# Kernel tuning notes

Hardware: AMD Instinct MI355X
Metric: run time of the kernel (lower is better)

The kernel has to match this reference:

```python
import jax, jax.numpy as jnp
import numpy as np

N, E, D, H = 50000, 500000, 128, 128


def setup_inputs() -> dict:
    key = jax.random.key(0)
    ks = jax.random.split(key, 20)
    s = 0.05
    inp = {
        "node_states": jax.random.normal(ks[0], (N, D), jnp.float32),
        "edge_features": jax.random.normal(ks[1], (E, D), jnp.float32),
        "from_idx": jax.random.randint(ks[2], (E,), 0, N, dtype=jnp.int32),
        "to_idx": jax.random.randint(ks[3], (E,), 0, N, dtype=jnp.int32),
        "graph_idx": jax.random.randint(ks[4], (N,), 0, 16, dtype=jnp.int32),
        # message MLP: Linear(3D,H)-ReLU-Linear(H,H)-ReLU-Linear(H,D)
        "mW1": jax.random.normal(ks[5], (3 * D, H), jnp.float32) * s,
        "mb1": jnp.zeros((H,), jnp.float32),
        "mW2": jax.random.normal(ks[6], (H, H), jnp.float32) * s,
        "mb2": jnp.zeros((H,), jnp.float32),
        "mW3": jax.random.normal(ks[7], (H, D), jnp.float32) * s,
        "mb3": jnp.zeros((D,), jnp.float32),
    }
    # three GRU cells; W: input->gates [D,3D], U: hidden->gates [D,3D]; gate order r,z,n (torch)
    for i, g in enumerate(["g0", "g1", "g2"]):
        inp[g + "W"] = jax.random.normal(ks[8 + 2 * i], (D, 3 * D), jnp.float32) * s
        inp[g + "U"] = jax.random.normal(ks[9 + 2 * i], (D, 3 * D), jnp.float32) * s
        inp[g + "b"] = jnp.zeros((3 * D,), jnp.float32)
        inp[g + "c"] = jnp.zeros((3 * D,), jnp.float32)
    return inp


def _mlp(x, W1, b1, W2, b2, W3, b3):
    h = jax.nn.relu(x @ W1 + b1)
    h = jax.nn.relu(h @ W2 + b2)
    return h @ W3 + b3


def _gru(x, h, W, U, b, c):
    gi = x @ W + b  # [N,3D]
    gh = h @ U + c
    ir, iz, inn = jnp.split(gi, 3, axis=1)
    hr, hz, hn = jnp.split(gh, 3, axis=1)
    r = jax.nn.sigmoid(ir + hr)
    z = jax.nn.sigmoid(iz + hz)
    n = jnp.tanh(inn + r * hn)
    return (1.0 - z) * n + z * h


def reference(node_states, edge_features, from_idx, to_idx, graph_idx,
              mW1, mb1, mW2, mb2, mW3, mb3,
              g0W, g0U, g0b, g0c, g1W, g1U, g1b, g1c, g2W, g2U, g2b, g2c):
    n_nodes = node_states.shape[0]

    def prop_once(fi, ti):
        edge_in = jnp.concatenate(
            [node_states[fi], node_states[ti], edge_features], axis=1)  # [E,3D]
        edge_states = _mlp(edge_in, mW1, mb1, mW2, mb2, mW3, mb3)  # [E,D]
        return jax.ops.segment_sum(edge_states, ti, num_segments=n_nodes)

    # forward uses self.message_net for BOTH directions (reverse net unused)
    agg = prop_once(from_idx, to_idx) + prop_once(to_idx, from_idx)  # [N,D]

    h1 = _gru(node_states, agg, g0W, g0U, g0b, g0c)
    h2 = _gru(agg, h1, g1W, g1U, g1b, g1c)
    h3 = _gru(h1, h2, g2W, g2U, g2b, g2c)
    return h3
```

## Files before the change

### kernel.cpp

```cpp
#include <hip/hip_runtime.h>

typedef unsigned short u16;
typedef __attribute__((ext_vector_type(8))) short bf16x8;
typedef __attribute__((ext_vector_type(4))) float f32x4;

__device__ inline u16 f2bf(float f) {
  unsigned int u = __float_as_uint(f);
  u += 0x7fffu + ((u >> 16) & 1u);
  return (u16)(u >> 16);
}
__device__ inline float bf2f(u16 v) {
  return __uint_as_float((unsigned)v << 16);
}

__device__ inline uint4 pack8(float4 a, float4 b) {
  uint4 r;
  r.x = (unsigned)f2bf(a.x) | ((unsigned)f2bf(a.y) << 16);
  r.y = (unsigned)f2bf(a.z) | ((unsigned)f2bf(a.w) << 16);
  r.z = (unsigned)f2bf(b.x) | ((unsigned)f2bf(b.y) << 16);
  r.w = (unsigned)f2bf(b.z) | ((unsigned)f2bf(b.w) << 16);
  return r;
}

__device__ inline void atomic_pk_add_bf16(u16* p, unsigned v) {
  asm volatile("global_atomic_pk_add_bf16 %0, %1, off" : : "v"(p), "v"(v)
               : "memory");
}

struct TransDesc {
  const float* src[9];
  u16* dst[9];
  int R[9];
  int C[9];
  int pre[10];
};

__global__ void transpose_all_kernel(TransDesc td) {
  int t = blockIdx.x * 256 + threadIdx.x;
  if (t >= td.pre[9]) return;
  int seg = 0;
  while (t >= td.pre[seg + 1]) ++seg;
  int local = t - td.pre[seg];
  int C = td.C[seg], R = td.R[seg];
  int r = local / C, c = local - r * C;
  td.dst[seg][(size_t)c * R + r] = f2bf(td.src[seg][local]);
}

__global__ void bf16_to_f32_kernel(const u16* __restrict__ in,
                                   float* __restrict__ out, int n8) {
  int t = blockIdx.x * 256 + threadIdx.x;
  if (t < n8) {
    uint4 v = ((const uint4*)in)[t];
    u16* p = (u16*)&v;
    float4 o0 = {bf2f(p[0]), bf2f(p[1]), bf2f(p[2]), bf2f(p[3])};
    float4 o1 = {bf2f(p[4]), bf2f(p[5]), bf2f(p[6]), bf2f(p[7])};
    ((float4*)out)[t * 2] = o0;
    ((float4*)out)[t * 2 + 1] = o1;
  }
}

__global__ void count_kernel(const int* __restrict__ fi,
                             const int* __restrict__ ti,
                             int* __restrict__ cnt, int E) {
  int e = blockIdx.x * 256 + threadIdx.x;
  if (e < E) {
    atomicAdd(&cnt[ti[e]], 1);
    atomicAdd(&cnt[fi[e]], 1);
  }
}

__global__ void scan1_kernel(const int* __restrict__ cnt,
                             int* __restrict__ partial, int N, int chunk) {
  __shared__ int sdata[256];
  int b = blockIdx.x, t = threadIdx.x;
  int base = b * chunk;
  int sum = 0;
  for (int i = t; i < chunk; i += 256) {
    int idx = base + i;
    if (idx < N) sum += cnt[idx];
  }
  sdata[t] = sum;
  __syncthreads();
  for (int s2 = 128; s2 > 0; s2 >>= 1) {
    if (t < s2) sdata[t] += sdata[t + s2];
    __syncthreads();
  }
  if (t == 0) partial[b] = sdata[0];
}

__global__ void scan2_kernel(int* __restrict__ partial, int* __restrict__ off,
                             int N) {
  __shared__ int s[256];
  int t = threadIdx.x;
  int own = partial[t];
  s[t] = own;
  __syncthreads();
  for (int d2 = 1; d2 < 256; d2 <<= 1) {
    int v = (t >= d2) ? s[t - d2] : 0;
    __syncthreads();
    s[t] += v;
    __syncthreads();
  }
  partial[t] = s[t] - own;
  if (t == 255) off[N] = s[255];
}

__global__ void scan3_kernel(const int* __restrict__ cnt,
                             const int* __restrict__ partialEx,
                             int* __restrict__ off, int* __restrict__ cursor,
                             int N, int chunk) {
  __shared__ int s[256];
  int b = blockIdx.x, t = threadIdx.x;
  int base = b * chunk;
  int own = (t < chunk && base + t < N) ? cnt[base + t] : 0;
  s[t] = own;
  __syncthreads();
  for (int d2 = 1; d2 < 256; d2 <<= 1) {
    int v = (t >= d2) ? s[t - d2] : 0;
    __syncthreads();
    s[t] += v;
    __syncthreads();
  }
  int ex = s[t] - own + partialEx[b];
  if (t < chunk && base + t < N) {
    off[base + t] = ex;
    cursor[base + t] = ex;
  }
}

__global__ void pos_kernel(const int* __restrict__ fi,
                           const int* __restrict__ ti, int* __restrict__ cursor,
                           int* __restrict__ pos0, int* __restrict__ pos1,
                           int E) {
  int e = blockIdx.x * 256 + threadIdx.x;
  if (e < E) {
    pos0[e] = atomicAdd(&cursor[ti[e]], 1);
    pos1[e] = atomicAdd(&cursor[fi[e]], 1);
  }
}

__global__ __launch_bounds__(256) void agg_csr_kernel(
    const u16* __restrict__ msg, const int* __restrict__ off,
    float* __restrict__ aggf, int N) {
  int n = blockIdx.x * 4 + (threadIdx.x >> 6);
  if (n >= N) return;
  int lane = threadIdx.x & 63;
  int s = off[n], e = off[n + 1];
  float a0 = 0.f, a1 = 0.f, b0 = 0.f, b1 = 0.f;
  const unsigned* m32 = (const unsigned*)msg;
  int r = s;
  for (; r + 1 < e; r += 2) {
    unsigned d0 = m32[(size_t)r * 64 + lane];
    unsigned d1 = m32[(size_t)(r + 1) * 64 + lane];
    a0 += bf2f((u16)(d0 & 0xffff));
    a1 += bf2f((u16)(d0 >> 16));
    b0 += bf2f((u16)(d1 & 0xffff));
    b1 += bf2f((u16)(d1 >> 16));
  }
  if (r < e) {
    unsigned d0 = m32[(size_t)r * 64 + lane];
    a0 += bf2f((u16)(d0 & 0xffff));
    a1 += bf2f((u16)(d0 >> 16));
  }
  aggf[(size_t)n * 128 + lane * 2] = a0 + b0;
  aggf[(size_t)n * 128 + lane * 2 + 1] = a1 + b1;
}

__device__ inline void stage_w_rw(u16* sW, const u16* __restrict__ src,
                                  int roww, int colofs, int tid) {
  int n = tid >> 1, half = tid & 1;
  const u16* s = src + (size_t)n * roww + colofs + half * 64;
#pragma unroll
  for (int q = 0; q < 8; ++q) {
    uint4 v = *(const uint4*)(s + q * 8);
    int byte = n * 256 + ((half * 128 + q * 16) ^ ((n & 7) << 4));
    *(uint4*)((char*)sW + byte) = v;
  }
}

__device__ inline void mfma_pass(const u16* A, const u16* W, f32x4 acc[8],
                                 int w, int lane) {
  const int cA = lane & 15;
  const int ko = (lane >> 4) * 8;
  const int arow = 16 * w + cA;
#pragma unroll
  for (int kk = 0; kk < 4; ++kk) {
    int ka = (kk * 32 + ko) * 2;
    int sx = ka ^ ((cA & 7) << 4);
    bf16x8 a = *(const bf16x8*)((const char*)A + arow * 256 + sx);
#pragma unroll
    for (int nt = 0; nt < 8; ++nt) {
      bf16x8 bb = *(const bf16x8*)((const char*)W + (nt * 16 + cA) * 256 + sx);
      acc[nt] = __builtin_amdgcn_mfma_f32_16x16x32_bf16(a, bb, acc[nt], 0, 0, 0);
    }
  }
}

__device__ inline void write_h_lds(u16* sH, const f32x4 acc[8], int w,
                                   int lane) {
#pragma unroll
  for (int nt = 0; nt < 8; ++nt) {
    int col = nt * 16 + (lane & 15);
#pragma unroll
    for (int i = 0; i < 4; ++i) {
      int rr = 16 * w + ((lane >> 4) * 4) + i;
      *(u16*)((char*)sH + rr * 256 + ((col * 2) ^ ((rr & 7) << 4))) =
          f2bf(acc[nt][i]);
    }
  }
}

__device__ inline void stage_w_512(u16* sW, const u16* __restrict__ src,
                                   int roww, int colofs, int tid) {
  int n = tid >> 2, quarter = tid & 3;
  const u16* s = src + (size_t)n * roww + colofs + quarter * 32;
#pragma unroll
  for (int q = 0; q < 4; ++q) {
    uint4 v = *(const uint4*)(s + q * 8);
    int byte = n * 256 + ((quarter * 64 + q * 16) ^ ((n & 7) << 4));
    *(uint4*)((char*)sW + byte) = v;
  }
}

__global__ __launch_bounds__(256) void node_partial_kernel(
    const float* __restrict__ ns, const u16* __restrict__ Wt1,
    u16* __restrict__ Pa, u16* __restrict__ Pb, int N) {
  __shared__ u16 sA[64 * 128];
  __shared__ u16 sW[128 * 128];
  const int tid = threadIdx.x;
  const int lane = tid & 63;
  const int w = tid >> 6;
  const int r0 = blockIdx.x * 64;
  {
    int row = tid >> 2, seg = tid & 3;
    int rr = r0 + row;
    if (rr >= N) rr = N - 1;
    const float4* sx = (const float4*)(ns + (size_t)rr * 128 + seg * 32);
#pragma unroll
    for (int q = 0; q < 4; ++q) {
      int byte = row * 256 + ((seg * 64 + q * 16) ^ ((row & 7) << 4));
      *(uint4*)((char*)sA + byte) = pack8(sx[q * 2], sx[q * 2 + 1]);
    }
  }
  stage_w_rw(sW, Wt1, 384, 0, tid);
  __syncthreads();
  f32x4 accA[8] = {};
  mfma_pass(sA, sW, accA, w, lane);
  __syncthreads();
  stage_w_rw(sW, Wt1, 384, 128, tid);
  __syncthreads();
  f32x4 accB[8] = {};
  mfma_pass(sA, sW, accB, w, lane);
#pragma unroll
  for (int nt = 0; nt < 8; ++nt) {
    int col = nt * 16 + (lane & 15);
#pragma unroll
    for (int i = 0; i < 4; ++i) {
      int rr = 16 * w + ((lane >> 4) * 4) + i;
      int row = r0 + rr;
      if (row < N) {
        Pa[(size_t)row * 128 + col] = f2bf(accA[nt][i]);
        Pb[(size_t)row * 128 + col] = f2bf(accB[nt][i]);
      }
    }
  }
}

template <int MODE>
__global__ __launch_bounds__(512, 2) void edge_fused_kernel(
    const float* __restrict__ ef, const int* __restrict__ from_idx,
    const int* __restrict__ to_idx, const u16* __restrict__ Wt1,
    const u16* __restrict__ Wt2, const u16* __restrict__ Wt3,
    const u16* __restrict__ Pa, const u16* __restrict__ Pb,
    const float* __restrict__ b1, const float* __restrict__ b2,
    const float* __restrict__ b3, const int* __restrict__ pos0,
    const int* __restrict__ pos1, u16* __restrict__ out_buf, int E,
    int ntiles) {
  __shared__ u16 sW1c[128 * 128];
  __shared__ u16 sH[128 * 128];
  __shared__ int sPos[128];
  const int tid = threadIdx.x;
  const int lane = tid & 63;
  const int wv = tid >> 6;
  const int mw = wv >> 1;
  const int nw = wv & 1;
  const int dir = mw >> 1;
  const int l15 = lane & 15;
  const int lhi = lane >> 4;

  stage_w_512(sW1c, Wt1, 384, 256, tid);

  float b1f[4], b2f[4], b3f[4];
#pragma unroll
  for (int nt = 0; nt < 4; ++nt) {
    int col = (nw << 6) + (nt << 4) + l15;
    b1f[nt] = b1[col];
    b2f[nt] = b2[col];
    b3f[nt] = b3[col];
  }
  bf16x8 w2f[4][4], w3f[4][4];
#pragma unroll
  for (int nt = 0; nt < 4; ++nt) {
    int c = (nw << 6) + (nt << 4) + l15;
#pragma unroll
    for (int kk = 0; kk < 4; ++kk) {
      w2f[nt][kk] = *(const bf16x8*)(Wt2 + (size_t)c * 128 + (kk << 5) + (lhi << 3));
      w3f[nt][kk] = *(const bf16x8*)(Wt3 + (size_t)c * 128 + (kk << 5) + (lhi << 3));
    }
  }
  __syncthreads();

  for (int t = blockIdx.x; t < ntiles; t += gridDim.x) {
    const int e0 = t << 6;
    if (MODE == 0 && tid < 128) {
      int er = tid & 63;
      int e = e0 + er;
      int p = -1;
      if (e < E) p = (tid < 64) ? pos0[e] : pos1[e];
      sPos[tid] = p;
    }
    {
      const int arow = (mw << 4) + l15;
      int e = e0 + arow;
      if (e >= E) e = E - 1;
      const float* ep = ef + (size_t)e * 128 + (lhi << 3);
      bf16x8 efA[4];
#pragma unroll
      for (int kk = 0; kk < 4; ++kk) {
        float4 f0 = *(const float4*)(ep + (kk << 5));
        float4 f1 = *(const float4*)(ep + (kk << 5) + 4);
        uint4 u = pack8(f0, f1);
        efA[kk] = *(bf16x8*)&u;
      }
      f32x4 a1[4] = {};
#pragma unroll
      for (int kk = 0; kk < 4; ++kk) {
#pragma unroll
        for (int nt = 0; nt < 4; ++nt) {
          int c = (nw << 6) + (nt << 4) + l15;
          int sx = ((kk << 6) + (lhi << 4)) ^ ((c & 7) << 4);
          bf16x8 bb = *(const bf16x8*)((const char*)sW1c + c * 256 + sx);
          a1[nt] = __builtin_amdgcn_mfma_f32_16x16x32_bf16(efA[kk], bb, a1[nt], 0, 0, 0);
        }
      }
#pragma unroll
      for (int nt = 0; nt < 4; ++nt) {
        int col = (nw << 6) + (nt << 4) + l15;
#pragma unroll
        for (int i = 0; i < 4; ++i) {
          int row = (mw << 4) + (lhi << 2) + i;
          u16 val = f2bf(a1[nt][i] + b1f[nt]);
          int sw = (col * 2) ^ ((row & 7) << 4);
          *(u16*)((char*)sH + row * 256 + sw) = val;
          *(u16*)((char*)sH + (row + 64) * 256 + sw) = val;
        }
      }
    }
    __syncthreads();
#pragma unroll
    for (int it = 0; it < 4; ++it) {
      int row = (tid >> 4) + (it << 5);
      int c8 = tid & 15;
      int er = row & 63, d = row >> 6;
      int ec = e0 + er;
      if (ec >= E) ec = E - 1;
      int fi_e = from_idx[ec], ti_e = to_idx[ec];
      int sA = d ? ti_e : fi_e;
      int sB = d ? fi_e : ti_e;
      char* hptr = (char*)sH + row * 256 + ((c8 << 4) ^ ((row & 7) << 4));
      uint4 efv = *(const uint4*)hptr;
      uint4 pav = *(const uint4*)(Pa + (size_t)sA * 128 + (c8 << 3));
      uint4 pbv = *(const uint4*)(Pb + (size_t)sB * 128 + (c8 << 3));
      const u16* pe = (const u16*)&efv;
      const u16* pa = (const u16*)&pav;
      const u16* pb = (const u16*)&pbv;
      unsigned o[4];
#pragma unroll
      for (int j = 0; j < 4; ++j) {
        float v0 = fmaxf(bf2f(pe[2 * j]) + bf2f(pa[2 * j]) + bf2f(pb[2 * j]), 0.f);
        float v1 = fmaxf(bf2f(pe[2 * j + 1]) + bf2f(pa[2 * j + 1]) + bf2f(pb[2 * j + 1]), 0.f);
        o[j] = (unsigned)f2bf(v0) | ((unsigned)f2bf(v1) << 16);
      }
      *(uint4*)hptr = *(uint4*)o;
    }
    __syncthreads();
    bf16x8 hA[2][4];
#pragma unroll
    for (int m = 0; m < 2; ++m) {
      int ra = (mw << 5) + (m << 4) + l15;
#pragma unroll
      for (int kk = 0; kk < 4; ++kk) {
        int sx = ((kk << 6) + (lhi << 4)) ^ ((ra & 7) << 4);
        hA[m][kk] = *(const bf16x8*)((const char*)sH + ra * 256 + sx);
      }
    }
    f32x4 acc2[2][4] = {};
#pragma unroll
    for (int kk = 0; kk < 4; ++kk)
#pragma unroll
      for (int nt = 0; nt < 4; ++nt)
#pragma unroll
        for (int m = 0; m < 2; ++m)
          acc2[m][nt] = __builtin_amdgcn_mfma_f32_16x16x32_bf16(
              hA[m][kk], w2f[nt][kk], acc2[m][nt], 0, 0, 0);
    __syncthreads();
#pragma unroll
    for (int m = 0; m < 2; ++m) {
#pragma unroll
      for (int i = 0; i < 4; ++i) {
        int rl = (mw << 5) + (m << 4) + (lhi << 2) + i;
#pragma unroll
        for (int nt = 0; nt < 4; ++nt) {
          int col = (nw << 6) + (nt << 4) + l15;
          float v = fmaxf(acc2[m][nt][i] + b2f[nt], 0.f);
          *(u16*)((char*)sH + rl * 256 + ((col * 2) ^ ((rl & 7) << 4))) = f2bf(v);
        }
      }
    }
    __syncthreads();
#pragma unroll
    for (int m = 0; m < 2; ++m) {
      int ra = (mw << 5) + (m << 4) + l15;
#pragma unroll
      for (int kk = 0; kk < 4; ++kk) {
        int sx = ((kk << 6) + (lhi << 4)) ^ ((ra & 7) << 4);
        hA[m][kk] = *(const bf16x8*)((const char*)sH + ra * 256 + sx);
      }
    }
    f32x4 acc3[2][4] = {};
#pragma unroll
    for (int kk = 0; kk < 4; ++kk)
#pragma unroll
      for (int nt = 0; nt < 4; ++nt)
#pragma unroll
        for (int m = 0; m < 2; ++m)
          acc3[m][nt] = __builtin_amdgcn_mfma_f32_16x16x32_bf16(
              hA[m][kk], w3f[nt][kk], acc3[m][nt], 0, 0, 0);

    if (MODE == 0) {
      __syncthreads();
#pragma unroll
      for (int m = 0; m < 2; ++m) {
#pragma unroll
        for (int i = 0; i < 4; ++i) {
          int rl = (mw << 5) + (m << 4) + (lhi << 2) + i;
#pragma unroll
          for (int nt = 0; nt < 4; ++nt) {
            int col = (nw << 6) + (nt << 4) + l15;
            *(u16*)((char*)sH + rl * 256 + ((col * 2) ^ ((rl & 7) << 4))) =
                f2bf(acc3[m][nt][i] + b3f[nt]);
          }
        }
      }
      __syncthreads();
#pragma unroll
      for (int it = 0; it < 4; ++it) {
        int task = tid + (it << 9);
        int row = task >> 4, c8 = task & 15;
        int p = sPos[row];
        if (p >= 0) {
          uint4 v = *(const uint4*)((const char*)sH + row * 256 +
                                    ((c8 << 4) ^ ((row & 7) << 4)));
          *(uint4*)(out_buf + (size_t)p * 128 + (c8 << 3)) = v;
        }
      }
      __syncthreads();
    } else {
#pragma unroll
      for (int m = 0; m < 2; ++m) {
#pragma unroll
        for (int i = 0; i < 4; ++i) {
          int er = ((mw & 1) << 5) + (m << 4) + (lhi << 2) + i;
          int e = e0 + er;
#pragma unroll
          for (int nt = 0; nt < 4; ++nt) {
            int col = (nw << 6) + (nt << 4) + l15;
            float v = acc3[m][nt][i] + b3f[nt];
            float vp = __shfl_xor(v, 1);
            if (e < E && !(lane & 1)) {
              int dest = dir ? from_idx[e] : to_idx[e];
              unsigned d2 = (unsigned)f2bf(v) | ((unsigned)f2bf(vp) << 16);
              atomic_pk_add_bf16(out_buf + (size_t)dest * 128 + col, d2);
            }
          }
        }
      }
      __syncthreads();
    }
  }
}

__global__ __launch_bounds__(256, 2) void gru3_kernel(
    const float* __restrict__ ns, const float* __restrict__ aggf,
    const u16* __restrict__ g0W, const u16* __restrict__ g0U,
    const u16* __restrict__ g1W, const u16* __restrict__ g1U,
    const u16* __restrict__ g2W, const u16* __restrict__ g2U,
    const float* __restrict__ b0, const float* __restrict__ c0,
    const float* __restrict__ b1, const float* __restrict__ c1,
    const float* __restrict__ b2, const float* __restrict__ c2,
    float* __restrict__ out, int N) {
  __shared__ u16 sX[64 * 128];
  __shared__ u16 sG[64 * 128];
  __shared__ u16 sW[128 * 128];
  const int tid = threadIdx.x;
  const int lane = tid & 63;
  const int w = tid >> 6;
  const int r0 = blockIdx.x * 64;
  {
    int row = tid >> 2, seg = tid & 3;
    int rr = r0 + row;
    if (rr >= N) rr = N - 1;
    const float4* sx = (const float4*)(ns + (size_t)rr * 128 + seg * 32);
    const float4* sh = (const float4*)(aggf + (size_t)rr * 128 + seg * 32);
#pragma unroll
    for (int q = 0; q < 4; ++q) {
      int byte = row * 256 + ((seg * 64 + q * 16) ^ ((row & 7) << 4));
      *(uint4*)((char*)sX + byte) = pack8(sx[q * 2], sx[q * 2 + 1]);
      *(uint4*)((char*)sG + byte) = pack8(sh[q * 2], sh[q * 2 + 1]);
    }
  }

  float hpf[8][4];

#define GPASS(SRC, ABUF, ACC)                       \
  __syncthreads();                                  \
  stage_w_rw(sW, (SRC), 128, 0, tid);               \
  __syncthreads();                                  \
  mfma_pass((ABUF), sW, (ACC), w, lane);

  {
    f32x4 ar[8] = {}, az[8] = {}, ai[8] = {}, ah[8] = {};
    GPASS(g0W + 0 * 16384, sX, ar)
    GPASS(g0U + 0 * 16384, sG, ar)
    GPASS(g0W + 1 * 16384, sX, az)
    GPASS(g0U + 1 * 16384, sG, az)
    GPASS(g0W + 2 * 16384, sX, ai)
    GPASS(g0U + 2 * 16384, sG, ah)
    f32x4 h1[8];
#pragma unroll
    for (int nt = 0; nt < 8; ++nt) {
      int col = nt * 16 + (lane & 15);
      float brc = b0[col] + c0[col];
      float bzc = b0[128 + col] + c0[128 + col];
      float bi = b0[256 + col];
      float bc2 = c0[256 + col];
#pragma unroll
      for (int i = 0; i < 4; ++i) {
        int rloc = 16 * w + ((lane >> 4) * 4) + i;
        int row = r0 + rloc;
        int rowc = row < N ? row : N - 1;
        float hf = aggf[(size_t)rowc * 128 + col];
        float rg = 1.f / (1.f + __expf(-(ar[nt][i] + brc)));
        float zg = 1.f / (1.f + __expf(-(az[nt][i] + bzc)));
        float pre = ai[nt][i] + bi + rg * (ah[nt][i] + bc2);
        float ng = 2.f / (1.f + __expf(-2.f * pre)) - 1.f;
        float hv = (1.f - zg) * ng + zg * hf;
        h1[nt][i] = hv;
        hpf[nt][i] = hv;
      }
    }
    write_h_lds(sX, h1, w, lane);
  }
  {
    f32x4 ar[8] = {}, az[8] = {}, ai[8] = {}, ah[8] = {};
    GPASS(g1W + 0 * 16384, sG, ar)
    GPASS(g1U + 0 * 16384, sX, ar)
    GPASS(g1W + 1 * 16384, sG, az)
    GPASS(g1U + 1 * 16384, sX, az)
    GPASS(g1W + 2 * 16384, sG, ai)
    GPASS(g1U + 2 * 16384, sX, ah)
    f32x4 h2[8];
#pragma unroll
    for (int nt = 0; nt < 8; ++nt) {
      int col = nt * 16 + (lane & 15);
      float brc = b1[col] + c1[col];
      float bzc = b1[128 + col] + c1[128 + col];
      float bi = b1[256 + col];
      float bc2 = c1[256 + col];
#pragma unroll
      for (int i = 0; i < 4; ++i) {
        float rg = 1.f / (1.f + __expf(-(ar[nt][i] + brc)));
        float zg = 1.f / (1.f + __expf(-(az[nt][i] + bzc)));
        float pre = ai[nt][i] + bi + rg * (ah[nt][i] + bc2);
        float ng = 2.f / (1.f + __expf(-2.f * pre)) - 1.f;
        float hv = (1.f - zg) * ng + zg * hpf[nt][i];
        h2[nt][i] = hv;
        hpf[nt][i] = hv;
      }
    }
    write_h_lds(sG, h2, w, lane);
  }
  {
    f32x4 ar[8] = {}, az[8] = {}, ai[8] = {}, ah[8] = {};
    GPASS(g2W + 0 * 16384, sX, ar)
    GPASS(g2U + 0 * 16384, sG, ar)
    GPASS(g2W + 1 * 16384, sX, az)
    GPASS(g2U + 1 * 16384, sG, az)
    GPASS(g2W + 2 * 16384, sX, ai)
    GPASS(g2U + 2 * 16384, sG, ah)
#pragma unroll
    for (int nt = 0; nt < 8; ++nt) {
      int col = nt * 16 + (lane & 15);
      float brc = b2[col] + c2[col];
      float bzc = b2[128 + col] + c2[128 + col];
      float bi = b2[256 + col];
      float bc2 = c2[256 + col];
#pragma unroll
      for (int i = 0; i < 4; ++i) {
        int rloc = 16 * w + ((lane >> 4) * 4) + i;
        int row = r0 + rloc;
        if (row < N) {
          float rg = 1.f / (1.f + __expf(-(ar[nt][i] + brc)));
          float zg = 1.f / (1.f + __expf(-(az[nt][i] + bzc)));
          float pre = ai[nt][i] + bi + rg * (ah[nt][i] + bc2);
          float ng = 2.f / (1.f + __expf(-2.f * pre)) - 1.f;
          out[(size_t)row * 128 + col] = (1.f - zg) * ng + zg * hpf[nt][i];
        }
      }
    }
  }
#undef GPASS
}

extern "C" void kernel_launch(void* const* d_in, const int* in_sizes, int n_in,
                              void* d_out, int out_size, void* d_ws,
                              size_t ws_size, hipStream_t stream) {
  const float* ns = (const float*)d_in[0];
  const float* ef = (const float*)d_in[1];
  const int* from_idx = (const int*)d_in[2];
  const int* to_idx = (const int*)d_in[3];
  const float* mW1 = (const float*)d_in[5];
  const float* mb1 = (const float*)d_in[6];
  const float* mW2 = (const float*)d_in[7];
  const float* mb2 = (const float*)d_in[8];
  const float* mW3 = (const float*)d_in[9];
  const float* mb3 = (const float*)d_in[10];
  const float* gW[3] = {(const float*)d_in[11], (const float*)d_in[15], (const float*)d_in[19]};
  const float* gU[3] = {(const float*)d_in[12], (const float*)d_in[16], (const float*)d_in[20]};
  const float* gb[3] = {(const float*)d_in[13], (const float*)d_in[17], (const float*)d_in[21]};
  const float* gc[3] = {(const float*)d_in[14], (const float*)d_in[18], (const float*)d_in[22]};

  const int N = in_sizes[0] / 128;
  const int E = in_sizes[1] / 128;

  char* base = (char*)d_ws;
  size_t cur = 0;
  auto alloc = [&](size_t bytes) {
    size_t p = cur;
    cur = (cur + bytes + 255) & ~(size_t)255;
    return (void*)(base + p);
  };
  float* aggf = (float*)alloc((size_t)N * 128 * 4);
  u16* Pa = (u16*)alloc((size_t)N * 128 * 2);
  u16* Pb = (u16*)alloc((size_t)N * 128 * 2);
  u16* Wt1 = (u16*)alloc(384 * 128 * 2);
  u16* Wt2 = (u16*)alloc(128 * 128 * 2);
  u16* Wt3 = (u16*)alloc(128 * 128 * 2);
  u16 *gWt[3], *gUt[3];
  for (int i = 0; i < 3; ++i) {
    gWt[i] = (u16*)alloc(384 * 128 * 2);
    gUt[i] = (u16*)alloc(384 * 128 * 2);
  }
  int* cnt = (int*)alloc((size_t)N * 4);
  int* off = (int*)alloc((size_t)(N + 1) * 4);
  int* cursor = (int*)alloc((size_t)N * 4);
  int* partial = (int*)alloc(256 * 4);
  int* pos0 = (int*)alloc((size_t)E * 4);
  int* pos1 = (int*)alloc((size_t)E * 4);
  u16* aggb = (u16*)alloc((size_t)N * 128 * 2);
  u16* msg = (u16*)alloc((size_t)2 * E * 128 * 2);
  bool csr_ok = (cur <= ws_size);

  {
    TransDesc td;
    const float* srcs[9] = {mW1, mW2, mW3, gW[0], gU[0], gW[1], gU[1], gW[2], gU[2]};
    u16* dsts[9] = {Wt1, Wt2, Wt3, gWt[0], gUt[0], gWt[1], gUt[1], gWt[2], gUt[2]};
    int Rs[9] = {384, 128, 128, 128, 128, 128, 128, 128, 128};
    int Cs[9] = {128, 128, 128, 384, 384, 384, 384, 384, 384};
    int acc = 0;
    for (int i = 0; i < 9; ++i) {
      td.src[i] = srcs[i];
      td.dst[i] = dsts[i];
      td.R[i] = Rs[i];
      td.C[i] = Cs[i];
      td.pre[i] = acc;
      acc += Rs[i] * Cs[i];
    }
    td.pre[9] = acc;
    transpose_all_kernel<<<(acc + 255) / 256, 256, 0, stream>>>(td);
  }

  node_partial_kernel<<<(N + 63) / 64, 256, 0, stream>>>(ns, Wt1, Pa, Pb, N);

  int ntiles = (E + 63) / 64;

  if (csr_ok) {
    hipMemsetAsync(cnt, 0, (size_t)N * 4, stream);
    count_kernel<<<(E + 255) / 256, 256, 0, stream>>>(from_idx, to_idx, cnt, E);
    int chunk = (N + 255) / 256;
    scan1_kernel<<<256, 256, 0, stream>>>(cnt, partial, N, chunk);
    scan2_kernel<<<1, 256, 0, stream>>>(partial, off, N);
    scan3_kernel<<<256, 256, 0, stream>>>(cnt, partial, off, cursor, N, chunk);
    pos_kernel<<<(E + 255) / 256, 256, 0, stream>>>(from_idx, to_idx, cursor,
                                                    pos0, pos1, E);
    int egrid = ntiles < 512 ? ntiles : 512;
    edge_fused_kernel<0><<<egrid, 512, 0, stream>>>(
        ef, from_idx, to_idx, Wt1, Wt2, Wt3, Pa, Pb, mb1, mb2, mb3, pos0, pos1,
        msg, E, ntiles);
    agg_csr_kernel<<<(N + 3) / 4, 256, 0, stream>>>(msg, off, aggf, N);
  } else {
    hipMemsetAsync(aggb, 0, (size_t)N * 128 * 2, stream);
    int egrid = ntiles < 512 ? ntiles : 512;
    edge_fused_kernel<1><<<egrid, 512, 0, stream>>>(
        ef, from_idx, to_idx, Wt1, Wt2, Wt3, Pa, Pb, mb1, mb2, mb3, pos0, pos1,
        aggb, E, ntiles);
    bf16_to_f32_kernel<<<(N * 16 + 255) / 256, 256, 0, stream>>>(aggb, aggf, N * 16);
  }

  int gblocks = (N + 63) / 64;
  gru3_kernel<<<gblocks, 256, 0, stream>>>(
      ns, aggf, gWt[0], gUt[0], gWt[1], gUt[1], gWt[2], gUt[2], gb[0], gc[0],
      gb[1], gc[1], gb[2], gc[2], (float*)d_out, N);
}
```

Before: 625.4 us.

## Process edges in destination-sorted slot order with segmented reduction and atomics

Replaces the edge-order fused MLP plus a separate 2E×128 message buffer and CSR gather kernel with a destination-sorted slot list. A separate GEMM precomputes the edge-feature part of layer 1 once per edge into a bf16 buffer. The edge kernel then processes 128 slots per tile and reduces runs of equal destination in LDS before issuing fp32 atomics into the aggregate. This drops the large message write/read and the aggregation pass, and also removes the low-memory fallback path. In exchange it adds random gathers of the precomputed edge rows, float atomics with nondeterministic summation order, and a memset of the aggregate.

```diff
diff --git a/kernel.cpp b/kernel.cpp
--- a/kernel.cpp
+++ b/kernel.cpp
@@ -20,11 +20,6 @@
   r.z = (unsigned)f2bf(b.x) | ((unsigned)f2bf(b.y) << 16);
   r.w = (unsigned)f2bf(b.z) | ((unsigned)f2bf(b.w) << 16);
   return r;
-}
-
-__device__ inline void atomic_pk_add_bf16(u16* p, unsigned v) {
-  asm volatile("global_atomic_pk_add_bf16 %0, %1, off" : : "v"(p), "v"(v)
-               : "memory");
 }
 
 struct TransDesc {
@@ -46,19 +41,6 @@
   td.dst[seg][(size_t)c * R + r] = f2bf(td.src[seg][local]);
 }
 
-__global__ void bf16_to_f32_kernel(const u16* __restrict__ in,
-                                   float* __restrict__ out, int n8) {
-  int t = blockIdx.x * 256 + threadIdx.x;
-  if (t < n8) {
-    uint4 v = ((const uint4*)in)[t];
-    u16* p = (u16*)&v;
-    float4 o0 = {bf2f(p[0]), bf2f(p[1]), bf2f(p[2]), bf2f(p[3])};
-    float4 o1 = {bf2f(p[4]), bf2f(p[5]), bf2f(p[6]), bf2f(p[7])};
-    ((float4*)out)[t * 2] = o0;
-    ((float4*)out)[t * 2 + 1] = o1;
-  }
-}
-
 __global__ void count_kernel(const int* __restrict__ fi,
                              const int* __restrict__ ti,
                              int* __restrict__ cnt, int E) {
@@ -88,8 +70,7 @@
   if (t == 0) partial[b] = sdata[0];
 }
 
-__global__ void scan2_kernel(int* __restrict__ partial, int* __restrict__ off,
-                             int N) {
+__global__ void scan2_kernel(int* __restrict__ partial) {
   __shared__ int s[256];
   int t = threadIdx.x;
   int own = partial[t];
@@ -102,13 +83,11 @@
     __syncthreads();
   }
   partial[t] = s[t] - own;
-  if (t == 255) off[N] = s[255];
 }
 
 __global__ void scan3_kernel(const int* __restrict__ cnt,
                              const int* __restrict__ partialEx,
-                             int* __restrict__ off, int* __restrict__ cursor,
-                             int N, int chunk) {
+                             int* __restrict__ cursor, int N, int chunk) {
   __shared__ int s[256];
   int b = blockIdx.x, t = threadIdx.x;
   int base = b * chunk;
@@ -122,48 +101,26 @@
     __syncthreads();
   }
   int ex = s[t] - own + partialEx[b];
-  if (t < chunk && base + t < N) {
-    off[base + t] = ex;
-    cursor[base + t] = ex;
-  }
-}
-
-__global__ void pos_kernel(const int* __restrict__ fi,
-                           const int* __restrict__ ti, int* __restrict__ cursor,
-                           int* __restrict__ pos0, int* __restrict__ pos1,
-                           int E) {
+  if (t < chunk && base + t < N) cursor[base + t] = ex;
+}
+
+__global__ void slot_kernel(const int* __restrict__ fi,
+                            const int* __restrict__ ti,
+                            int* __restrict__ cursor, int* __restrict__ s_nbr,
+                            int* __restrict__ s_eid, int* __restrict__ s_dest,
+                            int E) {
   int e = blockIdx.x * 256 + threadIdx.x;
   if (e < E) {
-    pos0[e] = atomicAdd(&cursor[ti[e]], 1);
-    pos1[e] = atomicAdd(&cursor[fi[e]], 1);
-  }
-}
-
-__global__ __launch_bounds__(256) void agg_csr_kernel(
-    const u16* __restrict__ msg, const int* __restrict__ off,
-    float* __restrict__ aggf, int N) {
-  int n = blockIdx.x * 4 + (threadIdx.x >> 6);
-  if (n >= N) return;
-  int lane = threadIdx.x & 63;
-  int s = off[n], e = off[n + 1];
-  float a0 = 0.f, a1 = 0.f, b0 = 0.f, b1 = 0.f;
-  const unsigned* m32 = (const unsigned*)msg;
-  int r = s;
-  for (; r + 1 < e; r += 2) {
-    unsigned d0 = m32[(size_t)r * 64 + lane];
-    unsigned d1 = m32[(size_t)(r + 1) * 64 + lane];
-    a0 += bf2f((u16)(d0 & 0xffff));
-    a1 += bf2f((u16)(d0 >> 16));
-    b0 += bf2f((u16)(d1 & 0xffff));
-    b1 += bf2f((u16)(d1 >> 16));
-  }
-  if (r < e) {
-    unsigned d0 = m32[(size_t)r * 64 + lane];
-    a0 += bf2f((u16)(d0 & 0xffff));
-    a1 += bf2f((u16)(d0 >> 16));
-  }
-  aggf[(size_t)n * 128 + lane * 2] = a0 + b0;
-  aggf[(size_t)n * 128 + lane * 2 + 1] = a1 + b1;
+    int f = fi[e], t2 = ti[e];
+    int p0 = atomicAdd(&cursor[t2], 1);
+    s_nbr[p0] = f;
+    s_eid[p0] = e;
+    s_dest[p0] = t2;
+    int p1 = atomicAdd(&cursor[f], 1);
+    s_nbr[p1] = t2;
+    s_eid[p1] = e;
+    s_dest[p1] = f;
+  }
 }
 
 __device__ inline void stage_w_rw(u16* sW, const u16* __restrict__ src,
@@ -207,18 +164,6 @@
       *(u16*)((char*)sH + rr * 256 + ((col * 2) ^ ((rr & 7) << 4))) =
           f2bf(acc[nt][i]);
     }
-  }
-}
-
-__device__ inline void stage_w_512(u16* sW, const u16* __restrict__ src,
-                                   int roww, int colofs, int tid) {
-  int n = tid >> 2, quarter = tid & 3;
-  const u16* s = src + (size_t)n * roww + colofs + quarter * 32;
-#pragma unroll
-  for (int q = 0; q < 4; ++q) {
-    uint4 v = *(const uint4*)(s + q * 8);
-    int byte = n * 256 + ((quarter * 64 + q * 16) ^ ((n & 7) << 4));
-    *(uint4*)((char*)sW + byte) = v;
   }
 }
 
@@ -266,35 +211,79 @@
   }
 }
 
-template <int MODE>
-__global__ __launch_bounds__(512, 2) void edge_fused_kernel(
-    const float* __restrict__ ef, const int* __restrict__ from_idx,
-    const int* __restrict__ to_idx, const u16* __restrict__ Wt1,
+__global__ __launch_bounds__(256) void efgemm_kernel(
+    const float* __restrict__ ef, const u16* __restrict__ Wt1,
+    const float* __restrict__ b1, u16* __restrict__ EFm, int E) {
+  __shared__ u16 sA[64 * 128];
+  __shared__ u16 sW[128 * 128];
+  const int tid = threadIdx.x;
+  const int lane = tid & 63;
+  const int w = tid >> 6;
+  const int r0 = blockIdx.x * 64;
+  {
+    int row = tid >> 2, seg = tid & 3;
+    int rr = r0 + row;
+    if (rr >= E) rr = E - 1;
+    const float4* sx = (const float4*)(ef + (size_t)rr * 128 + seg * 32);
+#pragma unroll
+    for (int q = 0; q < 4; ++q) {
+      int byte = row * 256 + ((seg * 64 + q * 16) ^ ((row & 7) << 4));
+      *(uint4*)((char*)sA + byte) = pack8(sx[q * 2], sx[q * 2 + 1]);
+    }
+  }
+  stage_w_rw(sW, Wt1, 384, 256, tid);
+  __syncthreads();
+  f32x4 acc[8] = {};
+  mfma_pass(sA, sW, acc, w, lane);
+  __syncthreads();
+#pragma unroll
+  for (int nt = 0; nt < 8; ++nt) {
+    int col = nt * 16 + (lane & 15);
+    float bv = b1[col];
+#pragma unroll
+    for (int i = 0; i < 4; ++i) {
+      int rr = 16 * w + ((lane >> 4) * 4) + i;
+      *(u16*)((char*)sA + rr * 256 + ((col * 2) ^ ((rr & 7) << 4))) =
+          f2bf(acc[nt][i] + bv);
+    }
+  }
+  __syncthreads();
+#pragma unroll
+  for (int it = 0; it < 4; ++it) {
+    int task = tid + (it << 8);
+    int row = task >> 4, c8 = task & 15;
+    int gr = r0 + row;
+    if (gr < E) {
+      uint4 v = *(const uint4*)((const char*)sA + row * 256 +
+                                ((c8 << 4) ^ ((row & 7) << 4)));
+      *(uint4*)(EFm + (size_t)gr * 128 + (c8 << 3)) = v;
+    }
+  }
+}
+
+__global__ __launch_bounds__(512, 2) void edge_csr_kernel(
+    const u16* __restrict__ EFm, const int* __restrict__ s_nbr,
+    const int* __restrict__ s_eid, const int* __restrict__ s_dest,
     const u16* __restrict__ Wt2, const u16* __restrict__ Wt3,
     const u16* __restrict__ Pa, const u16* __restrict__ Pb,
-    const float* __restrict__ b1, const float* __restrict__ b2,
-    const float* __restrict__ b3, const int* __restrict__ pos0,
-    const int* __restrict__ pos1, u16* __restrict__ out_buf, int E,
-    int ntiles) {
-  __shared__ u16 sW1c[128 * 128];
+    const float* __restrict__ b2, const float* __restrict__ b3,
+    float* __restrict__ aggf, int nslots, int ntiles) {
   __shared__ u16 sH[128 * 128];
-  __shared__ int sPos[128];
+  __shared__ int sNbr[128];
+  __shared__ int sEid[128];
+  __shared__ int sDest[128];
   const int tid = threadIdx.x;
   const int lane = tid & 63;
   const int wv = tid >> 6;
   const int mw = wv >> 1;
   const int nw = wv & 1;
-  const int dir = mw >> 1;
   const int l15 = lane & 15;
   const int lhi = lane >> 4;
 
-  stage_w_512(sW1c, Wt1, 384, 256, tid);
-
-  float b1f[4], b2f[4], b3f[4];
+  float b2f[4], b3f[4];
 #pragma unroll
   for (int nt = 0; nt < 4; ++nt) {
     int col = (nw << 6) + (nt << 4) + l15;
-    b1f[nt] = b1[col];
     b2f[nt] = b2[col];
     b3f[nt] = b3[col];
   }
@@ -311,66 +300,25 @@
   __syncthreads();
 
   for (int t = blockIdx.x; t < ntiles; t += gridDim.x) {
-    const int e0 = t << 6;
-    if (MODE == 0 && tid < 128) {
-      int er = tid & 63;
-      int e = e0 + er;
-      int p = -1;
-      if (e < E) p = (tid < 64) ? pos0[e] : pos1[e];
-      sPos[tid] = p;
-    }
-    {
-      const int arow = (mw << 4) + l15;
-      int e = e0 + arow;
-      if (e >= E) e = E - 1;
-      const float* ep = ef + (size_t)e * 128 + (lhi << 3);
-      bf16x8 efA[4];
-#pragma unroll
-      for (int kk = 0; kk < 4; ++kk) {
-        float4 f0 = *(const float4*)(ep + (kk << 5));
-        float4 f1 = *(const float4*)(ep + (kk << 5) + 4);
-        uint4 u = pack8(f0, f1);
-        efA[kk] = *(bf16x8*)&u;
-      }
-      f32x4 a1[4] = {};
-#pragma unroll
-      for (int kk = 0; kk < 4; ++kk) {
-#pragma unroll
-        for (int nt = 0; nt < 4; ++nt) {
-          int c = (nw << 6) + (nt << 4) + l15;
-          int sx = ((kk << 6) + (lhi << 4)) ^ ((c & 7) << 4);
-          bf16x8 bb = *(const bf16x8*)((const char*)sW1c + c * 256 + sx);
-          a1[nt] = __builtin_amdgcn_mfma_f32_16x16x32_bf16(efA[kk], bb, a1[nt], 0, 0, 0);
-        }
-      }
-#pragma unroll
-      for (int nt = 0; nt < 4; ++nt) {
-        int col = (nw << 6) + (nt << 4) + l15;
-#pragma unroll
-        for (int i = 0; i < 4; ++i) {
-          int row = (mw << 4) + (lhi << 2) + i;
-          u16 val = f2bf(a1[nt][i] + b1f[nt]);
-          int sw = (col * 2) ^ ((row & 7) << 4);
-          *(u16*)((char*)sH + row * 256 + sw) = val;
-          *(u16*)((char*)sH + (row + 64) * 256 + sw) = val;
-        }
-      }
+    const int r0 = t << 7;
+    if (tid < 128) {
+      int r = r0 + tid;
+      int rc = r < nslots ? r : nslots - 1;
+      sNbr[tid] = s_nbr[rc];
+      sEid[tid] = s_eid[rc];
+      sDest[tid] = (r < nslots) ? s_dest[rc] : -1;
     }
     __syncthreads();
 #pragma unroll
     for (int it = 0; it < 4; ++it) {
       int row = (tid >> 4) + (it << 5);
       int c8 = tid & 15;
-      int er = row & 63, d = row >> 6;
-      int ec = e0 + er;
-      if (ec >= E) ec = E - 1;
-      int fi_e = from_idx[ec], ti_e = to_idx[ec];
-      int sA = d ? ti_e : fi_e;
-      int sB = d ? fi_e : ti_e;
-      char* hptr = (char*)sH + row * 256 + ((c8 << 4) ^ ((row & 7) << 4));
-      uint4 efv = *(const uint4*)hptr;
-      uint4 pav = *(const uint4*)(Pa + (size_t)sA * 128 + (c8 << 3));
-      uint4 pbv = *(const uint4*)(Pb + (size_t)sB * 128 + (c8 << 3));
+      int nbr = sNbr[row], eid = sEid[row];
+      int dst = sDest[row];
+      if (dst < 0) dst = 0;
+      uint4 efv = *(const uint4*)(EFm + (size_t)eid * 128 + (c8 << 3));
+      uint4 pav = *(const uint4*)(Pa + (size_t)nbr * 128 + (c8 << 3));
+      uint4 pbv = *(const uint4*)(Pb + (size_t)dst * 128 + (c8 << 3));
       const u16* pe = (const u16*)&efv;
       const u16* pa = (const u16*)&pav;
       const u16* pb = (const u16*)&pbv;
@@ -381,7 +329,7 @@
         float v1 = fmaxf(bf2f(pe[2 * j + 1]) + bf2f(pa[2 * j + 1]) + bf2f(pb[2 * j + 1]), 0.f);
         o[j] = (unsigned)f2bf(v0) | ((unsigned)f2bf(v1) << 16);
       }
-      *(uint4*)hptr = *(uint4*)o;
+      *(uint4*)((char*)sH + row * 256 + ((c8 << 4) ^ ((row & 7) << 4))) = *(uint4*)o;
     }
     __syncthreads();
     bf16x8 hA[2][4];
@@ -436,57 +384,41 @@
         for (int m = 0; m < 2; ++m)
           acc3[m][nt] = __builtin_amdgcn_mfma_f32_16x16x32_bf16(
               hA[m][kk], w3f[nt][kk], acc3[m][nt], 0, 0, 0);
-
-    if (MODE == 0) {
-      __syncthreads();
-#pragma unroll
-      for (int m = 0; m < 2; ++m) {
-#pragma unroll
-        for (int i = 0; i < 4; ++i) {
-          int rl = (mw << 5) + (m << 4) + (lhi << 2) + i;
-#pragma unroll
-          for (int nt = 0; nt < 4; ++nt) {
-            int col = (nw << 6) + (nt << 4) + l15;
-            *(u16*)((char*)sH + rl * 256 + ((col * 2) ^ ((rl & 7) << 4))) =
-                f2bf(acc3[m][nt][i] + b3f[nt]);
-          }
+    __syncthreads();
+#pragma unroll
+    for (int m = 0; m < 2; ++m) {
+#pragma unroll
+      for (int i = 0; i < 4; ++i) {
+        int rl = (mw << 5) + (m << 4) + (lhi << 2) + i;
+#pragma unroll
+        for (int nt = 0; nt < 4; ++nt) {
+          int col = (nw << 6) + (nt << 4) + l15;
+          *(u16*)((char*)sH + rl * 256 + ((col * 2) ^ ((rl & 7) << 4))) =
+              f2bf(acc3[m][nt][i] + b3f[nt]);
         }
       }
-      __syncthreads();
-#pragma unroll
-      for (int it = 0; it < 4; ++it) {
-        int task = tid + (it << 9);
-        int row = task >> 4, c8 = task & 15;
-        int p = sPos[row];
-        if (p >= 0) {
-          uint4 v = *(const uint4*)((const char*)sH + row * 256 +
-                                    ((c8 << 4) ^ ((row & 7) << 4)));
-          *(uint4*)(out_buf + (size_t)p * 128 + (c8 << 3)) = v;
+    }
+    __syncthreads();
+    {
+      int c = tid & 127, q = tid >> 7;
+      float s = 0.f;
+      int prev = -1;
+      int rbeg = q << 5;
+#pragma unroll 4
+      for (int rr = rbeg; rr < rbeg + 32; ++rr) {
+        int d = sDest[rr];
+        if (d != prev) {
+          if (prev >= 0) unsafeAtomicAdd(&aggf[(size_t)prev * 128 + c], s);
+          prev = d;
+          s = 0.f;
         }
-      }
-      __syncthreads();
-    } else {
-#pragma unroll
-      for (int m = 0; m < 2; ++m) {
-#pragma unroll
-        for (int i = 0; i < 4; ++i) {
-          int er = ((mw & 1) << 5) + (m << 4) + (lhi << 2) + i;
-          int e = e0 + er;
-#pragma unroll
-          for (int nt = 0; nt < 4; ++nt) {
-            int col = (nw << 6) + (nt << 4) + l15;
-            float v = acc3[m][nt][i] + b3f[nt];
-            float vp = __shfl_xor(v, 1);
-            if (e < E && !(lane & 1)) {
-              int dest = dir ? from_idx[e] : to_idx[e];
-              unsigned d2 = (unsigned)f2bf(v) | ((unsigned)f2bf(vp) << 16);
-              atomic_pk_add_bf16(out_buf + (size_t)dest * 128 + col, d2);
-            }
-          }
-        }
-      }
-      __syncthreads();
-    }
+        if (d >= 0)
+          s += bf2f(*(const u16*)((const char*)sH + rr * 256 +
+                                  ((c * 2) ^ ((rr & 7) << 4))));
+      }
+      if (prev >= 0) unsafeAtomicAdd(&aggf[(size_t)prev * 128 + c], s);
+    }
+    __syncthreads();
   }
 }
 
@@ -642,6 +574,7 @@
 
   const int N = in_sizes[0] / 128;
   const int E = in_sizes[1] / 128;
+  const int nslots = 2 * E;
 
   char* base = (char*)d_ws;
   size_t cur = 0;
@@ -662,14 +595,13 @@
     gUt[i] = (u16*)alloc(384 * 128 * 2);
   }
   int* cnt = (int*)alloc((size_t)N * 4);
-  int* off = (int*)alloc((size_t)(N + 1) * 4);
   int* cursor = (int*)alloc((size_t)N * 4);
   int* partial = (int*)alloc(256 * 4);
-  int* pos0 = (int*)alloc((size_t)E * 4);
-  int* pos1 = (int*)alloc((size_t)E * 4);
-  u16* aggb = (u16*)alloc((size_t)N * 128 * 2);
-  u16* msg = (u16*)alloc((size_t)2 * E * 128 * 2);
-  bool csr_ok = (cur <= ws_size);
+  int* s_nbr = (int*)alloc((size_t)nslots * 4);
+  int* s_eid = (int*)alloc((size_t)nslots * 4);
+  int* s_dest = (int*)alloc((size_t)nslots * 4);
+  u16* EFm = (u16*)alloc((size_t)E * 128 * 2);
+  (void)ws_size;
 
   {
     TransDesc td;
@@ -692,30 +624,23 @@
 
   node_partial_kernel<<<(N + 63) / 64, 256, 0, stream>>>(ns, Wt1, Pa, Pb, N);
 
-  int ntiles = (E + 63) / 64;
-
-  if (csr_ok) {
-    hipMemsetAsync(cnt, 0, (size_t)N * 4, stream);
-    count_kernel<<<(E + 255) / 256, 256, 0, stream>>>(from_idx, to_idx, cnt, E);
-    int chunk = (N + 255) / 256;
-    scan1_kernel<<<256, 256, 0, stream>>>(cnt, partial, N, chunk);
-    scan2_kernel<<<1, 256, 0, stream>>>(partial, off, N);
-    scan3_kernel<<<256, 256, 0, stream>>>(cnt, partial, off, cursor, N, chunk);
-    pos_kernel<<<(E + 255) / 256, 256, 0, stream>>>(from_idx, to_idx, cursor,
-                                                    pos0, pos1, E);
-    int egrid = ntiles < 512 ? ntiles : 512;
-    edge_fused_kernel<0><<<egrid, 512, 0, stream>>>(
-        ef, from_idx, to_idx, Wt1, Wt2, Wt3, Pa, Pb, mb1, mb2, mb3, pos0, pos1,
-        msg, E, ntiles);
-    agg_csr_kernel<<<(N + 3) / 4, 256, 0, stream>>>(msg, off, aggf, N);
-  } else {
-    hipMemsetAsync(aggb, 0, (size_t)N * 128 * 2, stream);
-    int egrid = ntiles < 512 ? ntiles : 512;
-    edge_fused_kernel<1><<<egrid, 512, 0, stream>>>(
-        ef, from_idx, to_idx, Wt1, Wt2, Wt3, Pa, Pb, mb1, mb2, mb3, pos0, pos1,
-        aggb, E, ntiles);
-    bf16_to_f32_kernel<<<(N * 16 + 255) / 256, 256, 0, stream>>>(aggb, aggf, N * 16);
-  }
+  hipMemsetAsync(cnt, 0, (size_t)N * 4, stream);
+  count_kernel<<<(E + 255) / 256, 256, 0, stream>>>(from_idx, to_idx, cnt, E);
+  int chunk = (N + 255) / 256;
+  scan1_kernel<<<256, 256, 0, stream>>>(cnt, partial, N, chunk);
+  scan2_kernel<<<1, 256, 0, stream>>>(partial);
+  scan3_kernel<<<256, 256, 0, stream>>>(cnt, partial, cursor, N, chunk);
+  slot_kernel<<<(E + 255) / 256, 256, 0, stream>>>(from_idx, to_idx, cursor,
+                                                   s_nbr, s_eid, s_dest, E);
+
+  efgemm_kernel<<<(E + 63) / 64, 256, 0, stream>>>(ef, Wt1, mb1, EFm, E);
+
+  hipMemsetAsync(aggf, 0, (size_t)N * 128 * 4, stream);
+  int ntiles = (nslots + 127) / 128;
+  int egrid = ntiles < 512 ? ntiles : 512;
+  edge_csr_kernel<<<egrid, 512, 0, stream>>>(EFm, s_nbr, s_eid, s_dest, Wt2,
+                                             Wt3, Pa, Pb, mb2, mb3, aggf,
+                                             nslots, ntiles);
 
   int gblocks = (N + 63) / 64;
   gru3_kernel<<<gblocks, 256, 0, stream>>>(
```

Measured after the change: 648.9 us. 3.7% more time.
